# Kernel optimization log

Measured on AMD Instinct MI355X. Metric: run time of the kernel, lower is better.

The kernel has to match this reference:

```python
import jax, jax.numpy as jnp
import numpy as np

EPS = 1e-12
NEG = -1e30


def setup_inputs() -> dict:
    key = jax.random.key(0)
    ks = jax.random.split(key, 7)
    B, Nq, Lp, H, D = 96, 35, 180, 768, 128
    q_hidden = jax.random.normal(ks[0], (B, Nq, H), dtype=jnp.float32)
    pos_hidden = jax.random.normal(ks[1], (B, Lp, H), dtype=jnp.float32)
    neg_hidden = jax.random.normal(ks[2], (B, Lp, H), dtype=jnp.float32)
    W = jax.random.normal(ks[3], (H, D), dtype=jnp.float32) * 0.02
    b = jax.random.normal(ks[4], (D,), dtype=jnp.float32) * 0.02
    # non-punctuation filter mask; guarantee at least one valid token per passage
    pos_mask = jax.random.bernoulli(ks[5], 0.85, (B, Lp)).at[:, 0].set(True)
    neg_mask = jax.random.bernoulli(ks[6], 0.85, (B, Lp)).at[:, 0].set(True)
    return {"q_hidden": q_hidden, "pos_hidden": pos_hidden, "neg_hidden": neg_hidden,
            "W": W, "b": b, "pos_mask": pos_mask, "neg_mask": neg_mask}


def _vector_representation(h, W, b):
    # Linear projection then F.normalize(x) with torch default dim=1,
    # i.e. normalization over the SEQUENCE axis (faithful to source).
    x = jnp.einsum('blh,hd->bld', h, W) + b
    norm = jnp.maximum(jnp.sqrt(jnp.sum(x * x, axis=1, keepdims=True)), EPS)
    return x / norm


def _late_interaction(q, p, mask):
    # q: [Bq, Nq, D], p: [Bp, Lp, D], mask: [Bp, Lp] (True = keep token)
    sim = jnp.einsum('qnd,pld->qpnl', q, p)          # [Bq, Bp, Nq, Lp]
    sim = jnp.where(mask[None, :, None, :], sim, NEG)
    return jnp.max(sim, axis=-1).sum(axis=-1)        # MaxSim: max over Lp, sum over Nq


def reference(q_hidden, pos_hidden, neg_hidden, W, b, pos_mask, neg_mask):
    q = _vector_representation(q_hidden, W, b)
    pos = _vector_representation(pos_hidden, W, b)
    neg = _vector_representation(neg_hidden, W, b)
    pos_scores = _late_interaction(q, pos, pos_mask)
    neg_scores = _late_interaction(q, neg, neg_mask)
    return jnp.concatenate((pos_scores, neg_scores), axis=1)  # [B, 2B]
```

## Files before the change

kernel.cpp:

```cpp
#include <hip/hip_runtime.h>

typedef __attribute__((ext_vector_type(4))) float f32x4;
typedef __attribute__((ext_vector_type(8))) short s16x8;
typedef __attribute__((ext_vector_type(4))) short s16x4;
typedef __bf16 bf16x4 __attribute__((ext_vector_type(4)));

#define B_   96
#define NQ   35
#define LP   180
#define H_   768
#define D_   128
#define NEGF (-1e30f)

#define NROWS 37920
#define QROWS 3360
#define PROWS 17280

__device__ __forceinline__ unsigned short f2bf(float f) {
    return __builtin_bit_cast(unsigned short, (__bf16)f);
}

__device__ __forceinline__ s16x4 cvt_bf4(f32x4 v) {
    return __builtin_bit_cast(s16x4, __builtin_convertvector(v, bf16x4));
}

__device__ __forceinline__ s16x8 pack_bf16(f32x4 v0, f32x4 v1) {
    bf16x4 h0 = __builtin_convertvector(v0, bf16x4);
    bf16x4 h1 = __builtin_convertvector(v1, bf16x4);
    s16x4 a = __builtin_bit_cast(s16x4, h0), b = __builtin_bit_cast(s16x4, h1);
    return __builtin_shufflevector(a, b, 0, 1, 2, 3, 4, 5, 6, 7);
}

__device__ __forceinline__ void glds16(const void* g, void* l) {
    __builtin_amdgcn_global_load_lds(
        (const __attribute__((address_space(1))) unsigned int*)g,
        (__attribute__((address_space(3))) unsigned int*)l,
        16, 0, 0);
}

__global__ __launch_bounds__(256) void prep_k(
    const float* __restrict__ W, unsigned short* __restrict__ wthi,
    const unsigned int* __restrict__ pmask_w, unsigned int* __restrict__ ctrl,
    float* __restrict__ ssq) {
    __shared__ unsigned int rr[256];
    int b = blockIdx.x, t = threadIdx.x;
    if (b < 48) {
        int tid = b * 256 + t;
        int nt = tid / (24 * 64);
        int r = tid - nt * 24 * 64;
        int ks = r / 64, lane = r - ks * 64;
        int m = lane & 15, quad = lane >> 4;
        unsigned short* o = wthi + (size_t)tid * 8;
#pragma unroll
        for (int j = 0; j < 8; j++) {
            int k = ks * 32 + quad * 8 + j;
            o[j] = f2bf(W[(size_t)k * D_ + nt * 16 + m]);
        }
    } else if (b < 192) {
        ssq[(b - 48) * 256 + t] = 0.f;
    } else {
        unsigned int f1 = 0, f3 = 0, f4 = 0;
        for (int w = t; w < 4320; w += 256) {
            unsigned int v = pmask_w[w];
            f1 |= v & 0x0000ff00u;
            f3 |= v & 0xff000000u;
            if (w & 1) f4 |= v & 0x000000ffu;
        }
        rr[t] = f1; __syncthreads();
        for (int s2 = 128; s2; s2 >>= 1) { if (t < s2) rr[t] |= rr[t + s2]; __syncthreads(); }
        if (!t) ctrl[0] = rr[0];
        __syncthreads();
        rr[t] = f3; __syncthreads();
        for (int s2 = 128; s2; s2 >>= 1) { if (t < s2) rr[t] |= rr[t + s2]; __syncthreads(); }
        if (!t) ctrl[1] = rr[0];
        __syncthreads();
        rr[t] = f4; __syncthreads();
        for (int s2 = 128; s2; s2 >>= 1) { if (t < s2) rr[t] |= rr[t + s2]; __syncthreads(); }
        if (!t) ctrl[2] = rr[0];
    }
}

__global__ __launch_bounds__(256) void proj_k(
    const float* __restrict__ qh, const float* __restrict__ ph, const float* __restrict__ nh,
    const unsigned short* __restrict__ wthi, const float* __restrict__ bias,
    float* __restrict__ x, float* __restrict__ ssq,
    const void* __restrict__ pm, const void* __restrict__ nm,
    const unsigned int* __restrict__ ctrl, unsigned char* __restrict__ maskc) {
    __shared__ unsigned short sh[5120];
    int b = blockIdx.x;
    if (b >= 1185) {
        int i = (b - 1185) * 256 + threadIdx.x;
        const void* src = (i < B_ * LP) ? pm : nm;
        int j = (i < B_ * LP) ? i : i - B_ * LP;
        unsigned int c1 = ctrl[0], c3 = ctrl[1], c4 = ctrl[2];
        bool bit;
        if (c1 > 0)       bit = ((const unsigned char*)src)[j] != 0;
        else if (c3 > 0)  bit = ((const float*)src)[j] != 0.0f;
        else if (c4 > 0)  bit = ((const int*)src)[j] != 0;
        else              bit = ((const long long*)src)[j] != 0;
        maskc[i] = bit ? 1 : 0;
        return;
    }
    int t = threadIdx.x;
    int wave = t >> 6, lane = t & 63;
    const float* src; int row0l; int growbase;
    if (b < 105)      { src = qh; row0l = b * 32;         growbase = row0l; }
    else if (b < 645) { src = ph; row0l = (b - 105) * 32; growbase = QROWS + row0l; }
    else              { src = nh; row0l = (b - 645) * 32; growbase = QROWS + PROWS + row0l; }
    int m = lane & 15, quad = lane >> 4;

    int srow = t >> 4, c = t & 15;
    int sksg = c >> 3, kk = c & 7;
    int woff0 = sksg * 640 + srow * 40 + kk * 4;
    int woff1 = woff0 + 1280;
    int roff = m * 40 + quad * 8;
    const float* gp0 = src + (size_t)(row0l + srow) * H_ + c * 4;
    const float* gp1 = gp0 + (size_t)16 * H_;

    f32x4 acc[2][2];
#pragma unroll
    for (int mt = 0; mt < 2; mt++)
#pragma unroll
        for (int ntl = 0; ntl < 2; ntl++) acc[mt][ntl] = (f32x4){0.f, 0.f, 0.f, 0.f};

    int nt0 = wave * 2, nt1 = wave * 2 + 1;

    f32x4 pv0 = *(const f32x4*)gp0;
    f32x4 pv1 = *(const f32x4*)gp1;

#pragma unroll 2
    for (int s = 0; s < 12; s++) {
        int bufo = (s & 1) * 2560;
        *(s16x4*)&sh[bufo + woff0] = cvt_bf4(pv0);
        *(s16x4*)&sh[bufo + woff1] = cvt_bf4(pv1);
        __syncthreads();
        if (s < 11) {
            pv0 = *(const f32x4*)(gp0 + (s + 1) * 64);
            pv1 = *(const f32x4*)(gp1 + (s + 1) * 64);
        }
#pragma unroll
        for (int ksg = 0; ksg < 2; ksg++) {
            int ksgg = s * 2 + ksg;
            s16x8 a0 = *(const s16x8*)&sh[bufo + ksg * 640 + roff];
            s16x8 a1 = *(const s16x8*)&sh[bufo + ksg * 640 + 1280 + roff];
            s16x8 bh0 = *(const s16x8*)(wthi + ((size_t)(nt0 * 24 + ksgg) * 64 + lane) * 8);
            s16x8 bh1 = *(const s16x8*)(wthi + ((size_t)(nt1 * 24 + ksgg) * 64 + lane) * 8);
            acc[0][0] = __builtin_amdgcn_mfma_f32_16x16x32_bf16(a0, bh0, acc[0][0], 0, 0, 0);
            acc[0][1] = __builtin_amdgcn_mfma_f32_16x16x32_bf16(a0, bh1, acc[0][1], 0, 0, 0);
            acc[1][0] = __builtin_amdgcn_mfma_f32_16x16x32_bf16(a1, bh0, acc[1][0], 0, 0, 0);
            acc[1][1] = __builtin_amdgcn_mfma_f32_16x16x32_bf16(a1, bh1, acc[1][1], 0, 0, 0);
        }
    }

#pragma unroll
    for (int mt = 0; mt < 2; mt++) {
        int base = growbase + mt * 16;
        int bk0, bk1, b1start;
        if (base < QROWS)              { bk0 = base / 35;  bk1 = (base + 15) / 35;
                                         b1start = bk1 * 35; }
        else if (base < QROWS + PROWS) { int r0 = base - QROWS;
                                         bk0 = 96 + r0 / 180;  bk1 = 96 + (r0 + 15) / 180;
                                         b1start = QROWS + (bk1 - 96) * 180; }
        else                           { int r0 = base - QROWS - PROWS;
                                         bk0 = 192 + r0 / 180; bk1 = 192 + (r0 + 15) / 180;
                                         b1start = QROWS + PROWS + (bk1 - 192) * 180; }
#pragma unroll
        for (int ntl = 0; ntl < 2; ntl++) {
            int col = (wave * 2 + ntl) * 16 + m;
            float bv = bias[col];
            f32x4 s4 = acc[mt][ntl];
            float slo = 0.f, shi = 0.f;
#pragma unroll
            for (int r = 0; r < 4; r++) {
                int grow = base + quad * 4 + r;
                float v = s4[r] + bv;
                x[(size_t)grow * D_ + col] = v;
                float v2 = v * v;
                if (bk1 > bk0 && grow >= b1start) shi += v2; else slo += v2;
            }
            slo += __shfl_xor(slo, 16); slo += __shfl_xor(slo, 32);
            if (quad == 0) atomicAdd(ssq + (size_t)bk0 * D_ + col, slo);
            if (bk1 > bk0) {
                shi += __shfl_xor(shi, 16); shi += __shfl_xor(shi, 32);
                if (quad == 0) atomicAdd(ssq + (size_t)bk1 * D_ + col, shi);
            }
        }
    }
}

__global__ __launch_bounds__(256) void scatter_k(
    const float* __restrict__ x, const float* __restrict__ ssq,
    const unsigned char* __restrict__ maskc,
    unsigned short* __restrict__ qfrag, unsigned short* __restrict__ pfrag) {
    int c = blockIdx.x * 256 + threadIdx.x;
    int lane = c & 63, ks = (c >> 6) & 3;
    int quad = lane >> 4, mm = lane & 15;
    int d0 = ks * 32 + quad * 8;
    if (c < 61440) {
        int g = c >> 8;
        int mt = g % 5, qp = g / 5;
        int prow = mt * 16 + mm;
        s16x8 outv = (s16x8){0, 0, 0, 0, 0, 0, 0, 0};
        if (prow < 70) {
            int hi = prow >= 35;
            int bq = qp * 2 + hi;
            int l = prow - hi * 35;
            size_t row = (size_t)bq * 35 + l;
            const f32x4* px = (const f32x4*)(x + row * D_ + d0);
            f32x4 v0 = px[0], v1 = px[1];
            const f32x4* pq = (const f32x4*)(ssq + (size_t)bq * D_ + d0);
            f32x4 q0 = pq[0], q1 = pq[1];
            f32x4 r0, r1;
#pragma unroll
            for (int j = 0; j < 4; j++) {
                r0[j] = rsqrtf(fmaxf(q0[j], 1e-24f));
                r1[j] = rsqrtf(fmaxf(q1[j], 1e-24f));
            }
            outv = pack_bf16(v0 * r0, v1 * r1);
        }
        *(s16x8*)(qfrag + (size_t)c * 8) = outv;
    } else {
        int c2 = c - 61440;
        int g = c2 >> 8;
        int nt = g % 12, pbk = g / 12;
        int l = nt * 16 + mm;
        int lsrc = (l < LP && maskc[pbk * LP + l]) ? l : 0;
        size_t row = QROWS + (size_t)pbk * LP + lsrc;
        const f32x4* px = (const f32x4*)(x + row * D_ + d0);
        f32x4 v0 = px[0], v1 = px[1];
        const f32x4* pq = (const f32x4*)(ssq + (size_t)(96 + pbk) * D_ + d0);
        f32x4 q0 = pq[0], q1 = pq[1];
        f32x4 r0, r1;
#pragma unroll
        for (int j = 0; j < 4; j++) {
            r0[j] = rsqrtf(fmaxf(q0[j], 1e-24f));
            r1[j] = rsqrtf(fmaxf(q1[j], 1e-24f));
        }
        *(s16x8*)(pfrag + (size_t)c2 * 8) = pack_bf16(v0 * r0, v1 * r1);
    }
}

__global__ __launch_bounds__(256, 3) void interact_k(
    const unsigned short* __restrict__ qfrag, const unsigned short* __restrict__ pfrag,
    float* __restrict__ out) {
    __shared__ unsigned short plds[24576];
    int wave = threadIdx.x >> 6, lane = threadIdx.x & 63;
    int b = blockIdx.x;
    int xcd = b & 7, i = b >> 3;
    int c = xcd * 24 + (i % 24);
    int qg = i / 24;
    int side = c / 96, pb = c - side * 96;
    int qp = qg * 4 + wave;
    int m = lane & 15, quad = lane >> 4;

    const unsigned short* pbase = pfrag + (size_t)c * 24576;
    const unsigned short* qbase = qfrag + (size_t)qp * 10240;

#pragma unroll
    for (int ntl = 0; ntl < 3; ntl++) {
        int nt = wave * 3 + ntl;
#pragma unroll
        for (int ks = 0; ks < 4; ks++)
            glds16(pbase + ((size_t)(nt * 4 + ks) * 64 + lane) * 8,
                   &plds[(size_t)(nt * 4 + ks) * 512]);
    }

    s16x8 a[5][4];
#pragma unroll
    for (int mt = 0; mt < 5; mt++)
#pragma unroll
        for (int ks = 0; ks < 4; ks++)
            a[mt][ks] = *(const s16x8*)(qbase + ((size_t)(mt * 4 + ks) * 64 + lane) * 8);

    __syncthreads();

    const f32x4 zero4 = (f32x4){0.f, 0.f, 0.f, 0.f};
    float rmax[5][4];
#pragma unroll
    for (int mt = 0; mt < 5; mt++)
#pragma unroll
        for (int rr = 0; rr < 4; rr++) rmax[mt][rr] = NEGF;

    for (int nt = 0; nt < 12; nt++) {
        s16x8 bfr[4];
#pragma unroll
        for (int ks = 0; ks < 4; ks++)
            bfr[ks] = *(const s16x8*)&plds[((size_t)(nt * 4 + ks) * 64 + lane) * 8];
#pragma unroll
        for (int mt = 0; mt < 5; mt++) {
            f32x4 acc = __builtin_amdgcn_mfma_f32_16x16x32_bf16(a[mt][0], bfr[0], zero4, 0, 0, 0);
            acc = __builtin_amdgcn_mfma_f32_16x16x32_bf16(a[mt][1], bfr[1], acc, 0, 0, 0);
            acc = __builtin_amdgcn_mfma_f32_16x16x32_bf16(a[mt][2], bfr[2], acc, 0, 0, 0);
            acc = __builtin_amdgcn_mfma_f32_16x16x32_bf16(a[mt][3], bfr[3], acc, 0, 0, 0);
#pragma unroll
            for (int rr = 0; rr < 4; rr++)
                rmax[mt][rr] = fmaxf(rmax[mt][rr], acc[rr]);
        }
    }

#pragma unroll
    for (int mt = 0; mt < 5; mt++)
#pragma unroll
        for (int rr = 0; rr < 4; rr++) {
            float v = rmax[mt][rr];
            v = fmaxf(v, __shfl_xor(v, 1));
            v = fmaxf(v, __shfl_xor(v, 2));
            v = fmaxf(v, __shfl_xor(v, 4));
            v = fmaxf(v, __shfl_xor(v, 8));
            rmax[mt][rr] = v;
        }
    float s0 = 0.f, s1 = 0.f;
#pragma unroll
    for (int mt = 0; mt < 5; mt++)
#pragma unroll
        for (int rr = 0; rr < 4; rr++) {
            int prow = mt * 16 + quad * 4 + rr;
            float v = rmax[mt][rr];
            if (prow < 35) s0 += v;
            else if (prow < 70) s1 += v;
        }
    s0 += __shfl_xor(s0, 16); s0 += __shfl_xor(s0, 32);
    s1 += __shfl_xor(s1, 16); s1 += __shfl_xor(s1, 32);
    if (lane == 0) {
        int qb0 = qp * 2, qb1 = qp * 2 + 1;
        out[(size_t)qb0 * (2 * B_) + side * B_ + pb] = s0;
        out[(size_t)qb1 * (2 * B_) + side * B_ + pb] = s1;
    }
}

extern "C" void kernel_launch(void* const* d_in, const int* in_sizes, int n_in,
                              void* d_out, int out_size, void* d_ws, size_t ws_size,
                              hipStream_t stream) {
    const float* qh   = (const float*)d_in[0];
    const float* ph   = (const float*)d_in[1];
    const float* nh   = (const float*)d_in[2];
    const float* W    = (const float*)d_in[3];
    const float* bias = (const float*)d_in[4];
    const void* pmask = d_in[5];
    const void* nmask = d_in[6];
    float* out = (float*)d_out;
    char* ws = (char*)d_ws;

    constexpr size_t CTRL_OFF  = 0;
    constexpr size_t WTHI_OFF  = 256;
    constexpr size_t MASKC_OFF = WTHI_OFF + 196608;
    constexpr size_t SSQ_OFF   = 231424;
    constexpr size_t X_OFF     = SSQ_OFF + 147456;
    constexpr size_t QFRAG_OFF = X_OFF + (size_t)NROWS * D_ * 4;
    constexpr size_t PFRAG_OFF = QFRAG_OFF + 983040;

    unsigned int* ctrl     = (unsigned int*)(ws + CTRL_OFF);
    unsigned short* wthi   = (unsigned short*)(ws + WTHI_OFF);
    unsigned char* maskc   = (unsigned char*)(ws + MASKC_OFF);
    float* ssq             = (float*)(ws + SSQ_OFF);
    float* x               = (float*)(ws + X_OFF);
    unsigned short* qfrag  = (unsigned short*)(ws + QFRAG_OFF);
    unsigned short* pfrag  = (unsigned short*)(ws + PFRAG_OFF);

    prep_k<<<193, 256, 0, stream>>>(W, wthi, (const unsigned int*)pmask, ctrl, ssq);
    proj_k<<<1185 + 135, 256, 0, stream>>>(qh, ph, nh, wthi, bias, x, ssq,
                                           pmask, nmask, ctrl, maskc);
    scatter_k<<<2544, 256, 0, stream>>>(x, ssq, maskc, qfrag, pfrag);
    interact_k<<<2304, 256, 0, stream>>>(qfrag, pfrag, out);
}
```

Before: 198.0 us.

## Deepen projection prefetch, coalesce scatter via LDS, reuse passage tile across queries

The projection kernel now keeps a two-stage register prefetch of the hidden-state loads, so global latency is hidden further ahead. The scatter kernel stages each 16-row tile through shared memory, so its reads of x are row-contiguous and its fragment writes are linear, instead of gathering scattered 16-byte chunks per lane. The interaction kernel has each block loop over three query pairs per wave, reusing the LDS-resident passage tile. This cuts the grid from 2304 to 768 blocks and divides passage reloads by three, at the cost of fewer blocks to hide latency and more serial work per wave.

```diff
diff --git a/kernel.cpp b/kernel.cpp
--- a/kernel.cpp
+++ b/kernel.cpp
@@ -125,18 +125,21 @@
 
     int nt0 = wave * 2, nt1 = wave * 2 + 1;
 
-    f32x4 pv0 = *(const f32x4*)gp0;
-    f32x4 pv1 = *(const f32x4*)gp1;
+    f32x4 pvA0 = *(const f32x4*)gp0;
+    f32x4 pvA1 = *(const f32x4*)gp1;
+    f32x4 pvB0 = *(const f32x4*)(gp0 + 64);
+    f32x4 pvB1 = *(const f32x4*)(gp1 + 64);
 
 #pragma unroll 2
     for (int s = 0; s < 12; s++) {
         int bufo = (s & 1) * 2560;
-        *(s16x4*)&sh[bufo + woff0] = cvt_bf4(pv0);
-        *(s16x4*)&sh[bufo + woff1] = cvt_bf4(pv1);
+        *(s16x4*)&sh[bufo + woff0] = cvt_bf4(pvA0);
+        *(s16x4*)&sh[bufo + woff1] = cvt_bf4(pvA1);
         __syncthreads();
-        if (s < 11) {
-            pv0 = *(const f32x4*)(gp0 + (s + 1) * 64);
-            pv1 = *(const f32x4*)(gp1 + (s + 1) * 64);
+        pvA0 = pvB0; pvA1 = pvB1;
+        if (s < 10) {
+            pvB0 = *(const f32x4*)(gp0 + (s + 2) * 64);
+            pvB1 = *(const f32x4*)(gp1 + (s + 2) * 64);
         }
 #pragma unroll
         for (int ksg = 0; ksg < 2; ksg++) {
@@ -192,15 +195,16 @@
     const float* __restrict__ x, const float* __restrict__ ssq,
     const unsigned char* __restrict__ maskc,
     unsigned short* __restrict__ qfrag, unsigned short* __restrict__ pfrag) {
-    int c = blockIdx.x * 256 + threadIdx.x;
-    int lane = c & 63, ks = (c >> 6) & 3;
-    int quad = lane >> 4, mm = lane & 15;
-    int d0 = ks * 32 + quad * 8;
-    if (c < 61440) {
-        int g = c >> 8;
+    __shared__ unsigned short sh[16 * 136];
+    int g = blockIdx.x;
+    int t = threadIdx.x;
+    int srow = t >> 4, c16 = t & 15;
+    int d0 = c16 * 8;
+
+    s16x8 v8 = (s16x8){0, 0, 0, 0, 0, 0, 0, 0};
+    if (g < 240) {
         int mt = g % 5, qp = g / 5;
-        int prow = mt * 16 + mm;
-        s16x8 outv = (s16x8){0, 0, 0, 0, 0, 0, 0, 0};
+        int prow = mt * 16 + srow;
         if (prow < 70) {
             int hi = prow >= 35;
             int bq = qp * 2 + hi;
@@ -216,14 +220,12 @@
                 r0[j] = rsqrtf(fmaxf(q0[j], 1e-24f));
                 r1[j] = rsqrtf(fmaxf(q1[j], 1e-24f));
             }
-            outv = pack_bf16(v0 * r0, v1 * r1);
-        }
-        *(s16x8*)(qfrag + (size_t)c * 8) = outv;
+            v8 = pack_bf16(v0 * r0, v1 * r1);
+        }
     } else {
-        int c2 = c - 61440;
-        int g = c2 >> 8;
-        int nt = g % 12, pbk = g / 12;
-        int l = nt * 16 + mm;
+        int g2 = g - 240;
+        int nt = g2 % 12, pbk = g2 / 12;
+        int l = nt * 16 + srow;
         int lsrc = (l < LP && maskc[pbk * LP + l]) ? l : 0;
         size_t row = QROWS + (size_t)pbk * LP + lsrc;
         const f32x4* px = (const f32x4*)(x + row * D_ + d0);
@@ -236,8 +238,17 @@
             r0[j] = rsqrtf(fmaxf(q0[j], 1e-24f));
             r1[j] = rsqrtf(fmaxf(q1[j], 1e-24f));
         }
-        *(s16x8*)(pfrag + (size_t)c2 * 8) = pack_bf16(v0 * r0, v1 * r1);
-    }
+        v8 = pack_bf16(v0 * r0, v1 * r1);
+    }
+    *(s16x8*)&sh[srow * 136 + d0] = v8;
+    __syncthreads();
+
+    int ks = t >> 6, lane = t & 63;
+    int mm = lane & 15, quad = lane >> 4;
+    s16x8 o = *(const s16x8*)&sh[mm * 136 + ks * 32 + quad * 8];
+    unsigned short* dst = (g < 240) ? (qfrag + (size_t)g * 2048)
+                                    : (pfrag + (size_t)(g - 240) * 2048);
+    *(s16x8*)(dst + (size_t)t * 8) = o;
 }
 
 __global__ __launch_bounds__(256, 3) void interact_k(
@@ -250,11 +261,9 @@
     int c = xcd * 24 + (i % 24);
     int qg = i / 24;
     int side = c / 96, pb = c - side * 96;
-    int qp = qg * 4 + wave;
     int m = lane & 15, quad = lane >> 4;
 
     const unsigned short* pbase = pfrag + (size_t)c * 24576;
-    const unsigned short* qbase = qfrag + (size_t)qp * 10240;
 
 #pragma unroll
     for (int ntl = 0; ntl < 3; ntl++) {
@@ -264,67 +273,72 @@
             glds16(pbase + ((size_t)(nt * 4 + ks) * 64 + lane) * 8,
                    &plds[(size_t)(nt * 4 + ks) * 512]);
     }
-
-    s16x8 a[5][4];
-#pragma unroll
-    for (int mt = 0; mt < 5; mt++)
-#pragma unroll
-        for (int ks = 0; ks < 4; ks++)
-            a[mt][ks] = *(const s16x8*)(qbase + ((size_t)(mt * 4 + ks) * 64 + lane) * 8);
-
     __syncthreads();
 
     const f32x4 zero4 = (f32x4){0.f, 0.f, 0.f, 0.f};
-    float rmax[5][4];
-#pragma unroll
-    for (int mt = 0; mt < 5; mt++)
-#pragma unroll
-        for (int rr = 0; rr < 4; rr++) rmax[mt][rr] = NEGF;
-
-    for (int nt = 0; nt < 12; nt++) {
-        s16x8 bfr[4];
-#pragma unroll
-        for (int ks = 0; ks < 4; ks++)
-            bfr[ks] = *(const s16x8*)&plds[((size_t)(nt * 4 + ks) * 64 + lane) * 8];
-#pragma unroll
-        for (int mt = 0; mt < 5; mt++) {
-            f32x4 acc = __builtin_amdgcn_mfma_f32_16x16x32_bf16(a[mt][0], bfr[0], zero4, 0, 0, 0);
-            acc = __builtin_amdgcn_mfma_f32_16x16x32_bf16(a[mt][1], bfr[1], acc, 0, 0, 0);
-            acc = __builtin_amdgcn_mfma_f32_16x16x32_bf16(a[mt][2], bfr[2], acc, 0, 0, 0);
-            acc = __builtin_amdgcn_mfma_f32_16x16x32_bf16(a[mt][3], bfr[3], acc, 0, 0, 0);
-#pragma unroll
-            for (int rr = 0; rr < 4; rr++)
-                rmax[mt][rr] = fmaxf(rmax[mt][rr], acc[rr]);
-        }
-    }
-
-#pragma unroll
-    for (int mt = 0; mt < 5; mt++)
-#pragma unroll
-        for (int rr = 0; rr < 4; rr++) {
-            float v = rmax[mt][rr];
-            v = fmaxf(v, __shfl_xor(v, 1));
-            v = fmaxf(v, __shfl_xor(v, 2));
-            v = fmaxf(v, __shfl_xor(v, 4));
-            v = fmaxf(v, __shfl_xor(v, 8));
-            rmax[mt][rr] = v;
-        }
-    float s0 = 0.f, s1 = 0.f;
-#pragma unroll
-    for (int mt = 0; mt < 5; mt++)
-#pragma unroll
-        for (int rr = 0; rr < 4; rr++) {
-            int prow = mt * 16 + quad * 4 + rr;
-            float v = rmax[mt][rr];
-            if (prow < 35) s0 += v;
-            else if (prow < 70) s1 += v;
-        }
-    s0 += __shfl_xor(s0, 16); s0 += __shfl_xor(s0, 32);
-    s1 += __shfl_xor(s1, 16); s1 += __shfl_xor(s1, 32);
-    if (lane == 0) {
-        int qb0 = qp * 2, qb1 = qp * 2 + 1;
-        out[(size_t)qb0 * (2 * B_) + side * B_ + pb] = s0;
-        out[(size_t)qb1 * (2 * B_) + side * B_ + pb] = s1;
+
+    for (int qpi = 0; qpi < 3; qpi++) {
+        int qp = qg * 12 + wave * 3 + qpi;
+        const unsigned short* qbase = qfrag + (size_t)qp * 10240;
+
+        s16x8 a[5][4];
+#pragma unroll
+        for (int mt = 0; mt < 5; mt++)
+#pragma unroll
+            for (int ks = 0; ks < 4; ks++)
+                a[mt][ks] = *(const s16x8*)(qbase + ((size_t)(mt * 4 + ks) * 64 + lane) * 8);
+
+        float rmax[5][4];
+#pragma unroll
+        for (int mt = 0; mt < 5; mt++)
+#pragma unroll
+            for (int rr = 0; rr < 4; rr++) rmax[mt][rr] = NEGF;
+
+        for (int nt = 0; nt < 12; nt++) {
+            s16x8 bfr[4];
+#pragma unroll
+            for (int ks = 0; ks < 4; ks++)
+                bfr[ks] = *(const s16x8*)&plds[((size_t)(nt * 4 + ks) * 64 + lane) * 8];
+#pragma unroll
+            for (int mt = 0; mt < 5; mt++) {
+                f32x4 acc = __builtin_amdgcn_mfma_f32_16x16x32_bf16(a[mt][0], bfr[0], zero4, 0, 0, 0);
+                acc = __builtin_amdgcn_mfma_f32_16x16x32_bf16(a[mt][1], bfr[1], acc, 0, 0, 0);
+                acc = __builtin_amdgcn_mfma_f32_16x16x32_bf16(a[mt][2], bfr[2], acc, 0, 0, 0);
+                acc = __builtin_amdgcn_mfma_f32_16x16x32_bf16(a[mt][3], bfr[3], acc, 0, 0, 0);
+#pragma unroll
+                for (int rr = 0; rr < 4; rr++)
+                    rmax[mt][rr] = fmaxf(rmax[mt][rr], acc[rr]);
+            }
+        }
+
+#pragma unroll
+        for (int mt = 0; mt < 5; mt++)
+#pragma unroll
+            for (int rr = 0; rr < 4; rr++) {
+                float v = rmax[mt][rr];
+                v = fmaxf(v, __shfl_xor(v, 1));
+                v = fmaxf(v, __shfl_xor(v, 2));
+                v = fmaxf(v, __shfl_xor(v, 4));
+                v = fmaxf(v, __shfl_xor(v, 8));
+                rmax[mt][rr] = v;
+            }
+        float s0 = 0.f, s1 = 0.f;
+#pragma unroll
+        for (int mt = 0; mt < 5; mt++)
+#pragma unroll
+            for (int rr = 0; rr < 4; rr++) {
+                int prow = mt * 16 + quad * 4 + rr;
+                float v = rmax[mt][rr];
+                if (prow < 35) s0 += v;
+                else if (prow < 70) s1 += v;
+            }
+        s0 += __shfl_xor(s0, 16); s0 += __shfl_xor(s0, 32);
+        s1 += __shfl_xor(s1, 16); s1 += __shfl_xor(s1, 32);
+        if (lane == 0) {
+            int qb0 = qp * 2, qb1 = qp * 2 + 1;
+            out[(size_t)qb0 * (2 * B_) + side * B_ + pb] = s0;
+            out[(size_t)qb1 * (2 * B_) + side * B_ + pb] = s1;
+        }
     }
 }
 
@@ -361,5 +375,5 @@
     proj_k<<<1185 + 135, 256, 0, stream>>>(qh, ph, nh, wthi, bias, x, ssq,
                                            pmask, nmask, ctrl, maskc);
     scatter_k<<<2544, 256, 0, stream>>>(x, ssq, maskc, qfrag, pfrag);
-    interact_k<<<2304, 256, 0, stream>>>(qfrag, pfrag, out);
-}
+    interact_k<<<768, 256, 0, stream>>>(qfrag, pfrag, out);
+}
```

Result: slower. 262.0 us (+32.3%).
